# Optimization experiments

Hardware: AMD Instinct MI355X
Metric: run time of the kernel (lower is better)

## Reference

```python
import jax, jax.numpy as jnp
import numpy as np

D = 4096          # input_dim == output_dim (square FAUST factors)
N = 1024          # batch rows of U
NNZ = 131072      # nonzeros per factor (32 per row)
K = 4             # number of sparse factors


def setup_inputs() -> dict:
    key = jax.random.key(0)
    k_u, k_b, k_v, k_r, k_c = jax.random.split(key, 5)
    U = jax.random.normal(k_u, (N, D), dtype=jnp.float32)
    bias = jax.random.normal(k_b, (D,), dtype=jnp.float32)
    # glorot-ish scaling: ~32 nnz per row -> scale by 1/sqrt(32) for stable chain
    vals = jax.random.normal(k_v, (K, NNZ), dtype=jnp.float32) * (1.0 / np.sqrt(32.0))
    rows = jax.random.randint(k_r, (K, NNZ), 0, D, dtype=jnp.int32)
    cols = jax.random.randint(k_c, (K, NNZ), 0, D, dtype=jnp.int32)
    return {"U": U, "bias": bias, "vals": vals, "rows": rows, "cols": cols}


def _spmm(rows, cols, vals, X):
    # sparse (COO) [D, D] @ dense X [D, N] -> [D, N]
    return jax.ops.segment_sum(vals[:, None] * X[cols], rows, num_segments=D)


def reference(U, bias, vals, rows, cols):
    # torch code applies sparse_matrices[-1] first, then [k-2] ... [0]
    y = U.T  # [D, N]
    for i in range(K - 1, -1, -1):
        y = _spmm(rows[i], cols[i], vals[i], y)
    return y.T + bias  # [N, D]
```

## Files before the change

### kernel.cpp

```cpp
#include <hip/hip_runtime.h>

#define D_DIM 4096
#define N_DIM 1024
#define NNZ_F 131072
#define K_F 4
#define NCHUNK 8
#define LPR 16
#define RPB 16
#define MAXE 1024
#define SEGE 512
#define XS8 (N_DIM / 8)

#define T_TILES ((D_DIM / 64) * (N_DIM / 64))
#define TSTRIDE 132

__device__ __forceinline__ unsigned short f2bf(float f) {
    union { float f; unsigned int u; } v; v.f = f;
    unsigned int r = v.u + 0x7fffu + ((v.u >> 16) & 1u);
    return (unsigned short)(r >> 16);
}
__device__ __forceinline__ float bf_lo(unsigned int w) {
    return __uint_as_float(w << 16);
}
__device__ __forceinline__ float bf_hi_raw(unsigned int w) {
    return __uint_as_float(w);
}

__global__ __launch_bounds__(1024) void fused_t_build_k(const float* __restrict__ in,
                                                        unsigned short* __restrict__ outb,
                                                        const int* __restrict__ rows,
                                                        int* __restrict__ row_ptr_g,
                                                        int* __restrict__ cursor_g,
                                                        int* __restrict__ srow_g) {
    __shared__ int s_cnt[4 * D_DIM];
    __shared__ int s_part[1024];
    const int tid = threadIdx.x;
    const int bid = blockIdx.x;

    if (bid >= K_F) {
        const int tb = bid - K_F;
        float (*tile)[65] = (float (*)[65])s_cnt;
        const int gxi = tb & 63;
        const int gyi = tb >> 6;
        const int c0 = gxi * 64;
        const int r0 = gyi * 64;
        const int tx = tid & 63;
        const int ty = tid >> 6;
#pragma unroll
        for (int i = ty; i < 64; i += 16)
            tile[i][tx] = in[(size_t)(r0 + i) * D_DIM + c0 + tx];
        __syncthreads();
        const int px = (tid & 15) * 4;
        const int py = tid >> 4;
        ushort4 w;
        w.x = f2bf(tile[px + 0][py]);
        w.y = f2bf(tile[px + 1][py]);
        w.z = f2bf(tile[px + 2][py]);
        w.w = f2bf(tile[px + 3][py]);
        *(ushort4*)&outb[(size_t)(c0 + py) * N_DIM + r0 + px] = w;
        return;
    }

    const int f = bid;
    const int grp = (tid >> 8) & 3;
#pragma unroll
    for (int k = 0; k < 16; ++k) s_cnt[tid + k * 1024] = 0;
    __syncthreads();

    int* h = s_cnt + grp * D_DIM;
    const int4* rp4 = (const int4*)(rows + (size_t)f * NNZ_F);
#pragma unroll 4
    for (int it = 0; it < NNZ_F / 4096; ++it) {
        int4 r4 = rp4[(size_t)it * 1024 + tid];
        atomicAdd(&h[r4.x], 1);
        atomicAdd(&h[r4.y], 1);
        atomicAdd(&h[r4.z], 1);
        atomicAdd(&h[r4.w], 1);
    }
    __syncthreads();

    int c[4];
#pragma unroll
    for (int k = 0; k < 4; ++k)
        c[k] = s_cnt[tid * 4 + k] + s_cnt[D_DIM + tid * 4 + k]
             + s_cnt[2 * D_DIM + tid * 4 + k] + s_cnt[3 * D_DIM + tid * 4 + k];
    const int b = tid * 4;

    int* rp   = row_ptr_g + (size_t)f * (D_DIM + 1);
    int* cur  = cursor_g + (size_t)f * D_DIM;
    int* srow = srow_g + (size_t)f * D_DIM;

    if (f == 0) {
        const int part = c[0] + c[1] + c[2] + c[3];
        s_part[tid] = part;
        __syncthreads();
        for (int off = 1; off < 1024; off <<= 1) {
            int v = (tid >= off) ? s_part[tid - off] : 0;
            __syncthreads();
            s_part[tid] += v;
            __syncthreads();
        }
        int excl = s_part[tid] - part;
#pragma unroll
        for (int k = 0; k < 4; ++k) {
            rp[b + k] = excl; cur[b + k] = excl; srow[b + k] = b + k; excl += c[k];
        }
        if (tid == 1023) rp[D_DIM] = NNZ_F;
        return;
    }

    __syncthreads();
    int* hist = s_cnt + 4096;
    int* binc = s_cnt + 4352;
    int* sA   = s_cnt + 4608;
    int* sB   = s_cnt + 4864;
    if (tid < 256) { hist[tid] = 0; binc[tid] = 0; }
    __syncthreads();
#pragma unroll
    for (int k = 0; k < 4; ++k) {
        int l = c[k] > 255 ? 255 : c[k];
        atomicAdd(&hist[l], 1);
    }
    __syncthreads();
    if (tid < 256) { int hv = hist[tid]; sA[tid] = hv; sB[tid] = hv * tid; }
    __syncthreads();
    for (int off = 1; off < 256; off <<= 1) {
        int a = 0, bb = 0;
        if (tid < 256 && tid >= off) { a = sA[tid - off]; bb = sB[tid - off]; }
        __syncthreads();
        if (tid < 256) { sA[tid] += a; sB[tid] += bb; }
        __syncthreads();
    }
#pragma unroll
    for (int k = 0; k < 4; ++k) {
        const int l = c[k] > 255 ? 255 : c[k];
        const int idx = atomicAdd(&binc[l], 1);
        const int pos    = sA[l] - hist[l] + idx;
        const int startp = sB[l] - hist[l] * l + idx * l;
        srow[pos] = b + k;
        rp[pos] = startp;
        cur[b + k] = startp;
    }
    if (tid == 1023) rp[D_DIM] = NNZ_F;
}

__global__ __launch_bounds__(1024) void scatter_all_k(const int* __restrict__ rows,
                                                      const int* __restrict__ cols,
                                                      const float* __restrict__ vals,
                                                      int* __restrict__ cursor,
                                                      uint2* __restrict__ csr) {
    const int f = blockIdx.x >> 5;
    const size_t q = (size_t)(blockIdx.x & 31) * 1024 + threadIdx.x;
    const size_t base = (size_t)f * NNZ_F;
    const int4   r4 = ((const int4*)(rows + base))[q];
    const int4   c4 = ((const int4*)(cols + base))[q];
    const float4 v4 = ((const float4*)(vals + base))[q];
    int* curf = cursor + (size_t)f * D_DIM;
    int p;
    p = atomicAdd(&curf[r4.x], 1);
    csr[base + p] = make_uint2((unsigned)c4.x << 11, __float_as_uint(v4.x));
    p = atomicAdd(&curf[r4.y], 1);
    csr[base + p] = make_uint2((unsigned)c4.y << 11, __float_as_uint(v4.y));
    p = atomicAdd(&curf[r4.z], 1);
    csr[base + p] = make_uint2((unsigned)c4.z << 11, __float_as_uint(v4.z));
    p = atomicAdd(&curf[r4.w], 1);
    csr[base + p] = make_uint2((unsigned)c4.w << 11, __float_as_uint(v4.w));
}

template <bool FINAL>
__global__ __launch_bounds__(256) void spmm_chunk_k(const int* __restrict__ row_ptr,
                                                    const int* __restrict__ sorted_rows,
                                                    const uint2* __restrict__ csr,
                                                    const char* __restrict__ Xb,
                                                    uint4* __restrict__ Y,
                                                    float* __restrict__ out,
                                                    const float* __restrict__ bias) {
    constexpr int SMEM_BYTES = FINAL ? (16 * TSTRIDE * 4) : (4 * SEGE * 8);
    __shared__ __align__(16) char smem_raw[SMEM_BYTES];

    const int tid   = threadIdx.x;
    const int chunk = blockIdx.x & (NCHUNK - 1);
    const int rg    = blockIdx.x >> 3;
    const int lane  = tid & 15;
    const int slot  = chunk * LPR + lane;
    const unsigned sl16 = (unsigned)slot * 16u;

    float acc[8];
#pragma unroll
    for (int k = 0; k < 8; ++k) acc[k] = 0.f;

    if (!FINAL) {
        uint2 (*seg)[SEGE] = (uint2(*)[SEGE])smem_raw;
        const int wid  = tid >> 6;
        const int wl   = tid & 63;
        const int sub4 = (tid >> 4) & 3;
        int q;
        switch (wid) {
            case 0:  q = rg;        break;
            case 1:  q = 511 - rg;  break;
            case 2:  q = 512 + rg;  break;
            default: q = 1023 - rg; break;
        }
        const int qb    = q * 4;
        const int qs    = row_ptr[qb];
        const int qe    = row_ptr[qb + 4];
        const int start = row_ptr[qb + sub4];
        const int end_  = row_ptr[qb + sub4 + 1];
        const int r     = sorted_rows[qb + sub4];
        const int total = qe - qs;

        if (total <= SEGE) {
            for (int t = wl; t < total; t += 64)
                seg[wid][t] = csr[qs + t];
            asm volatile("s_waitcnt lgkmcnt(0)" ::: "memory");
            const uint2* sp = seg[wid];
            int j = start - qs;
            const int je = end_ - qs;
#pragma unroll 2
            for (; j + 1 < je; j += 2) {
                const uint2 e0 = sp[j];
                const uint2 e1 = sp[j + 1];
                const uint4 x0 = *(const uint4*)(Xb + (e0.x + sl16));
                const uint4 x1 = *(const uint4*)(Xb + (e1.x + sl16));
                const float v0 = __uint_as_float(e0.y);
                const float v1 = __uint_as_float(e1.y);
                acc[0] += v0 * bf_lo(x0.x); acc[1] += v0 * bf_hi_raw(x0.x);
                acc[2] += v0 * bf_lo(x0.y); acc[3] += v0 * bf_hi_raw(x0.y);
                acc[4] += v0 * bf_lo(x0.z); acc[5] += v0 * bf_hi_raw(x0.z);
                acc[6] += v0 * bf_lo(x0.w); acc[7] += v0 * bf_hi_raw(x0.w);
                acc[0] += v1 * bf_lo(x1.x); acc[1] += v1 * bf_hi_raw(x1.x);
                acc[2] += v1 * bf_lo(x1.y); acc[3] += v1 * bf_hi_raw(x1.y);
                acc[4] += v1 * bf_lo(x1.z); acc[5] += v1 * bf_hi_raw(x1.z);
                acc[6] += v1 * bf_lo(x1.w); acc[7] += v1 * bf_hi_raw(x1.w);
            }
            if (j < je) {
                const uint2 e0 = sp[j];
                const uint4 x0 = *(const uint4*)(Xb + (e0.x + sl16));
                const float v0 = __uint_as_float(e0.y);
                acc[0] += v0 * bf_lo(x0.x); acc[1] += v0 * bf_hi_raw(x0.x);
                acc[2] += v0 * bf_lo(x0.y); acc[3] += v0 * bf_hi_raw(x0.y);
                acc[4] += v0 * bf_lo(x0.z); acc[5] += v0 * bf_hi_raw(x0.z);
                acc[6] += v0 * bf_lo(x0.w); acc[7] += v0 * bf_hi_raw(x0.w);
            }
        } else {
            for (int j = start; j < end_; ++j) {
                const uint2 e0 = csr[j];
                const uint4 x0 = *(const uint4*)(Xb + (e0.x + sl16));
                const float v0 = __uint_as_float(e0.y);
                acc[0] += v0 * bf_lo(x0.x); acc[1] += v0 * bf_hi_raw(x0.x);
                acc[2] += v0 * bf_lo(x0.y); acc[3] += v0 * bf_hi_raw(x0.y);
                acc[4] += v0 * bf_lo(x0.z); acc[5] += v0 * bf_hi_raw(x0.z);
                acc[6] += v0 * bf_lo(x0.w); acc[7] += v0 * bf_hi_raw(x0.w);
            }
        }

        uint4 o;
        o.x = (unsigned int)f2bf(acc[0]) | ((unsigned int)f2bf(acc[1]) << 16);
        o.y = (unsigned int)f2bf(acc[2]) | ((unsigned int)f2bf(acc[3]) << 16);
        o.z = (unsigned int)f2bf(acc[4]) | ((unsigned int)f2bf(acc[5]) << 16);
        o.w = (unsigned int)f2bf(acc[6]) | ((unsigned int)f2bf(acc[7]) << 16);
        Y[(size_t)r * XS8 + slot] = o;
        return;
    }

    float* smem   = (float*)smem_raw;
    uint2* s_ent  = (uint2*)smem_raw;
    int*   s_ptr  = (int*)smem_raw + 2048;
    int*   s_srow = (int*)smem_raw + 2072;

    const int r0  = rg * RPB;
    const int sub = tid >> 4;

    if (tid <= RPB) s_ptr[tid] = row_ptr[r0 + tid];
    if (tid < RPB)  s_srow[tid] = sorted_rows[r0 + tid];
    __syncthreads();
    const int base  = s_ptr[0];
    const int total = s_ptr[RPB] - base;
    const int start = s_ptr[sub] - base;
    const int end_  = s_ptr[sub + 1] - base;
    const int r     = s_srow[sub];

    for (int cb2 = 0; cb2 < total; cb2 += MAXE) {
        int cnt = total - cb2;
        if (cnt > MAXE) cnt = MAXE;
        for (int t = tid; t < cnt; t += 256)
            s_ent[t] = csr[base + cb2 + t];
        __syncthreads();
        const int js = start > cb2 ? start : cb2;
        const int je = end_ < cb2 + cnt ? end_ : cb2 + cnt;
        int j = js;
#pragma unroll 2
        for (; j + 1 < je; j += 2) {
            const int j0 = j - cb2;
            const uint2 e0 = s_ent[j0];
            const uint2 e1 = s_ent[j0 + 1];
            const uint4 x0 = *(const uint4*)(Xb + (e0.x + sl16));
            const uint4 x1 = *(const uint4*)(Xb + (e1.x + sl16));
            const float v0 = __uint_as_float(e0.y);
            const float v1 = __uint_as_float(e1.y);
            acc[0] += v0 * bf_lo(x0.x); acc[1] += v0 * bf_hi_raw(x0.x);
            acc[2] += v0 * bf_lo(x0.y); acc[3] += v0 * bf_hi_raw(x0.y);
            acc[4] += v0 * bf_lo(x0.z); acc[5] += v0 * bf_hi_raw(x0.z);
            acc[6] += v0 * bf_lo(x0.w); acc[7] += v0 * bf_hi_raw(x0.w);
            acc[0] += v1 * bf_lo(x1.x); acc[1] += v1 * bf_hi_raw(x1.x);
            acc[2] += v1 * bf_lo(x1.y); acc[3] += v1 * bf_hi_raw(x1.y);
            acc[4] += v1 * bf_lo(x1.z); acc[5] += v1 * bf_hi_raw(x1.z);
            acc[6] += v1 * bf_lo(x1.w); acc[7] += v1 * bf_hi_raw(x1.w);
        }
        if (j < je) {
            const int j0 = j - cb2;
            const uint2 e0 = s_ent[j0];
            const uint4 x0 = *(const uint4*)(Xb + (e0.x + sl16));
            const float v0 = __uint_as_float(e0.y);
            acc[0] += v0 * bf_lo(x0.x); acc[1] += v0 * bf_hi_raw(x0.x);
            acc[2] += v0 * bf_lo(x0.y); acc[3] += v0 * bf_hi_raw(x0.y);
            acc[4] += v0 * bf_lo(x0.z); acc[5] += v0 * bf_hi_raw(x0.z);
            acc[6] += v0 * bf_lo(x0.w); acc[7] += v0 * bf_hi_raw(x0.w);
        }
        __syncthreads();
    }

    __syncthreads();
    float* tile = smem;
    const int wbase = sub * TSTRIDE + lane * 8;
    *(float4*)&tile[wbase]     = make_float4(acc[0], acc[1], acc[2], acc[3]);
    *(float4*)&tile[wbase + 4] = make_float4(acc[4], acc[5], acc[6], acc[7]);
    __syncthreads();
    const int n0 = chunk * (N_DIM / NCHUNK);
#pragma unroll
    for (int t = tid; t < 512; t += 256) {
        const int n_loc = t >> 2;
        const int qd    = t & 3;
        float4 o;
        o.x = tile[(qd * 4 + 0) * TSTRIDE + n_loc];
        o.y = tile[(qd * 4 + 1) * TSTRIDE + n_loc];
        o.z = tile[(qd * 4 + 2) * TSTRIDE + n_loc];
        o.w = tile[(qd * 4 + 3) * TSTRIDE + n_loc];
        const float4 bv = *(const float4*)&bias[r0 + qd * 4];
        o.x += bv.x; o.y += bv.y; o.z += bv.z; o.w += bv.w;
        *(float4*)&out[(size_t)(n0 + n_loc) * D_DIM + r0 + qd * 4] = o;
    }
}

extern "C" void kernel_launch(void* const* d_in, const int* in_sizes, int n_in,
                              void* d_out, int out_size, void* d_ws, size_t ws_size,
                              hipStream_t stream) {
    const float* U    = (const float*)d_in[0];
    const float* bias = (const float*)d_in[1];
    const float* vals = (const float*)d_in[2];
    const int*   rows = (const int*)d_in[3];
    const int*   cols = (const int*)d_in[4];
    float* out = (float*)d_out;

    char* ws = (char*)d_ws;
    size_t off = 0;
    char* bufA = ws;                   off += (size_t)D_DIM * N_DIM * 2;
    char* bufB = ws + off;             off += (size_t)D_DIM * N_DIM * 2;
    int* row_ptr = (int*)(ws + off);   off += (size_t)K_F * (D_DIM + 1) * 4;
    off = (off + 15) & ~(size_t)15;
    int* cursor  = (int*)(ws + off);   off += (size_t)K_F * D_DIM * 4;
    int* srow    = (int*)(ws + off);   off += (size_t)K_F * D_DIM * 4;
    off = (off + 15) & ~(size_t)15;
    uint2* csr   = (uint2*)(ws + off); off += (size_t)K_F * NNZ_F * 8;

    const int grid_spmm = (D_DIM / RPB) * NCHUNK;

    fused_t_build_k<<<T_TILES + K_F, 1024, 0, stream>>>(
        U, (unsigned short*)bufA, rows, row_ptr, cursor, srow);

    scatter_all_k<<<K_F * (NNZ_F / 4096), 1024, 0, stream>>>(rows, cols, vals, cursor, csr);

    spmm_chunk_k<false><<<grid_spmm, 256, 0, stream>>>(
        row_ptr + 3 * (D_DIM + 1), srow + 3 * D_DIM, csr + 3 * (size_t)NNZ_F,
        (const char*)bufA, (uint4*)bufB, nullptr, nullptr);
    spmm_chunk_k<false><<<grid_spmm, 256, 0, stream>>>(
        row_ptr + 2 * (D_DIM + 1), srow + 2 * D_DIM, csr + 2 * (size_t)NNZ_F,
        (const char*)bufB, (uint4*)bufA, nullptr, nullptr);
    spmm_chunk_k<false><<<grid_spmm, 256, 0, stream>>>(
        row_ptr + 1 * (D_DIM + 1), srow + 1 * D_DIM, csr + 1 * (size_t)NNZ_F,
        (const char*)bufA, (uint4*)bufB, nullptr, nullptr);
    spmm_chunk_k<true><<<grid_spmm, 256, 0, stream>>>(
        row_ptr + 0 * (D_DIM + 1), srow + 0 * D_DIM, csr + 0 * (size_t)NNZ_F,
        (const char*)bufB, nullptr, out, bias);
}
```

Before: 105.0 us.

## Balance final SpMM by length-sorting factor 0 quads and reuse per-wave path

Factor 0's row_ptr build now bins each group of four rows by its total length and writes the groups in length-sorted order, as the other factors already do, instead of keeping natural row order. This lets the final SpMM use the same per-wave, quad-paired, block-barrier-free path as the intermediate stages, replacing the block-wide chunked shared-memory loop with its __syncthreads. The final output is transposed through per-wave shared memory and written with the bias added for the four consecutive original rows (d0 = r - sub4). This relies on the sorted rows within a quad staying contiguous and aligned, and adds a histogram and scan step to factor 0's setup.

```diff
diff --git a/kernel.cpp b/kernel.cpp
--- a/kernel.cpp
+++ b/kernel.cpp
@@ -7,12 +7,10 @@
 #define NCHUNK 8
 #define LPR 16
 #define RPB 16
-#define MAXE 1024
 #define SEGE 512
 #define XS8 (N_DIM / 8)
 
 #define T_TILES ((D_DIM / 64) * (N_DIM / 64))
-#define TSTRIDE 132
 
 __device__ __forceinline__ unsigned short f2bf(float f) {
     union { float f; unsigned int u; } v; v.f = f;
@@ -33,7 +31,6 @@
                                                         int* __restrict__ cursor_g,
                                                         int* __restrict__ srow_g) {
     __shared__ int s_cnt[4 * D_DIM];
-    __shared__ int s_part[1024];
     const int tid = threadIdx.x;
     const int bid = blockIdx.x;
 
@@ -89,27 +86,42 @@
     int* rp   = row_ptr_g + (size_t)f * (D_DIM + 1);
     int* cur  = cursor_g + (size_t)f * D_DIM;
     int* srow = srow_g + (size_t)f * D_DIM;
+    __syncthreads();
 
     if (f == 0) {
-        const int part = c[0] + c[1] + c[2] + c[3];
-        s_part[tid] = part;
-        __syncthreads();
-        for (int off = 1; off < 1024; off <<= 1) {
-            int v = (tid >= off) ? s_part[tid - off] : 0;
+        int* hist = s_cnt + 4096;
+        int* binc = s_cnt + 4608;
+        int* sA   = s_cnt + 5120;
+        int* sB   = s_cnt + 5632;
+        if (tid < 512) { hist[tid] = 0; binc[tid] = 0; }
+        __syncthreads();
+        const int qlen = c[0] + c[1] + c[2] + c[3];
+        const int l = qlen > 511 ? 511 : qlen;
+        atomicAdd(&hist[l], 1);
+        __syncthreads();
+        if (tid < 512) { int hv = hist[tid]; sA[tid] = hv; sB[tid] = hv * tid; }
+        __syncthreads();
+        for (int off = 1; off < 512; off <<= 1) {
+            int a = 0, bb = 0;
+            if (tid < 512 && tid >= off) { a = sA[tid - off]; bb = sB[tid - off]; }
             __syncthreads();
-            s_part[tid] += v;
+            if (tid < 512) { sA[tid] += a; sB[tid] += bb; }
             __syncthreads();
         }
-        int excl = s_part[tid] - part;
+        const int idx = atomicAdd(&binc[l], 1);
+        const int pos = sA[l] - hist[l] + idx;
+        int pref = sB[l] - hist[l] * l + idx * l;
 #pragma unroll
         for (int k = 0; k < 4; ++k) {
-            rp[b + k] = excl; cur[b + k] = excl; srow[b + k] = b + k; excl += c[k];
+            rp[pos * 4 + k] = pref;
+            srow[pos * 4 + k] = b + k;
+            cur[b + k] = pref;
+            pref += c[k];
         }
         if (tid == 1023) rp[D_DIM] = NNZ_F;
         return;
     }
 
-    __syncthreads();
     int* hist = s_cnt + 4096;
     int* binc = s_cnt + 4352;
     int* sA   = s_cnt + 4608;
@@ -175,8 +187,7 @@
                                                     uint4* __restrict__ Y,
                                                     float* __restrict__ out,
                                                     const float* __restrict__ bias) {
-    constexpr int SMEM_BYTES = FINAL ? (16 * TSTRIDE * 4) : (4 * SEGE * 8);
-    __shared__ __align__(16) char smem_raw[SMEM_BYTES];
+    __shared__ __align__(16) uint2 seg[4][SEGE];
 
     const int tid   = threadIdx.x;
     const int chunk = blockIdx.x & (NCHUNK - 1);
@@ -184,116 +195,40 @@
     const int lane  = tid & 15;
     const int slot  = chunk * LPR + lane;
     const unsigned sl16 = (unsigned)slot * 16u;
+    const int wid  = tid >> 6;
+    const int wl   = tid & 63;
+    const int sub4 = (tid >> 4) & 3;
+
+    int q;
+    switch (wid) {
+        case 0:  q = rg;        break;
+        case 1:  q = 511 - rg;  break;
+        case 2:  q = 512 + rg;  break;
+        default: q = 1023 - rg; break;
+    }
+    const int qb    = q * 4;
+    const int qs    = row_ptr[qb];
+    const int qe    = row_ptr[qb + 4];
+    const int start = row_ptr[qb + sub4];
+    const int end_  = row_ptr[qb + sub4 + 1];
+    const int r     = sorted_rows[qb + sub4];
+    const int total = qe - qs;
 
     float acc[8];
 #pragma unroll
     for (int k = 0; k < 8; ++k) acc[k] = 0.f;
 
-    if (!FINAL) {
-        uint2 (*seg)[SEGE] = (uint2(*)[SEGE])smem_raw;
-        const int wid  = tid >> 6;
-        const int wl   = tid & 63;
-        const int sub4 = (tid >> 4) & 3;
-        int q;
-        switch (wid) {
-            case 0:  q = rg;        break;
-            case 1:  q = 511 - rg;  break;
-            case 2:  q = 512 + rg;  break;
-            default: q = 1023 - rg; break;
-        }
-        const int qb    = q * 4;
-        const int qs    = row_ptr[qb];
-        const int qe    = row_ptr[qb + 4];
-        const int start = row_ptr[qb + sub4];
-        const int end_  = row_ptr[qb + sub4 + 1];
-        const int r     = sorted_rows[qb + sub4];
-        const int total = qe - qs;
-
-        if (total <= SEGE) {
-            for (int t = wl; t < total; t += 64)
-                seg[wid][t] = csr[qs + t];
-            asm volatile("s_waitcnt lgkmcnt(0)" ::: "memory");
-            const uint2* sp = seg[wid];
-            int j = start - qs;
-            const int je = end_ - qs;
-#pragma unroll 2
-            for (; j + 1 < je; j += 2) {
-                const uint2 e0 = sp[j];
-                const uint2 e1 = sp[j + 1];
-                const uint4 x0 = *(const uint4*)(Xb + (e0.x + sl16));
-                const uint4 x1 = *(const uint4*)(Xb + (e1.x + sl16));
-                const float v0 = __uint_as_float(e0.y);
-                const float v1 = __uint_as_float(e1.y);
-                acc[0] += v0 * bf_lo(x0.x); acc[1] += v0 * bf_hi_raw(x0.x);
-                acc[2] += v0 * bf_lo(x0.y); acc[3] += v0 * bf_hi_raw(x0.y);
-                acc[4] += v0 * bf_lo(x0.z); acc[5] += v0 * bf_hi_raw(x0.z);
-                acc[6] += v0 * bf_lo(x0.w); acc[7] += v0 * bf_hi_raw(x0.w);
-                acc[0] += v1 * bf_lo(x1.x); acc[1] += v1 * bf_hi_raw(x1.x);
-                acc[2] += v1 * bf_lo(x1.y); acc[3] += v1 * bf_hi_raw(x1.y);
-                acc[4] += v1 * bf_lo(x1.z); acc[5] += v1 * bf_hi_raw(x1.z);
-                acc[6] += v1 * bf_lo(x1.w); acc[7] += v1 * bf_hi_raw(x1.w);
-            }
-            if (j < je) {
-                const uint2 e0 = sp[j];
-                const uint4 x0 = *(const uint4*)(Xb + (e0.x + sl16));
-                const float v0 = __uint_as_float(e0.y);
-                acc[0] += v0 * bf_lo(x0.x); acc[1] += v0 * bf_hi_raw(x0.x);
-                acc[2] += v0 * bf_lo(x0.y); acc[3] += v0 * bf_hi_raw(x0.y);
-                acc[4] += v0 * bf_lo(x0.z); acc[5] += v0 * bf_hi_raw(x0.z);
-                acc[6] += v0 * bf_lo(x0.w); acc[7] += v0 * bf_hi_raw(x0.w);
-            }
-        } else {
-            for (int j = start; j < end_; ++j) {
-                const uint2 e0 = csr[j];
-                const uint4 x0 = *(const uint4*)(Xb + (e0.x + sl16));
-                const float v0 = __uint_as_float(e0.y);
-                acc[0] += v0 * bf_lo(x0.x); acc[1] += v0 * bf_hi_raw(x0.x);
-                acc[2] += v0 * bf_lo(x0.y); acc[3] += v0 * bf_hi_raw(x0.y);
-                acc[4] += v0 * bf_lo(x0.z); acc[5] += v0 * bf_hi_raw(x0.z);
-                acc[6] += v0 * bf_lo(x0.w); acc[7] += v0 * bf_hi_raw(x0.w);
-            }
-        }
-
-        uint4 o;
-        o.x = (unsigned int)f2bf(acc[0]) | ((unsigned int)f2bf(acc[1]) << 16);
-        o.y = (unsigned int)f2bf(acc[2]) | ((unsigned int)f2bf(acc[3]) << 16);
-        o.z = (unsigned int)f2bf(acc[4]) | ((unsigned int)f2bf(acc[5]) << 16);
-        o.w = (unsigned int)f2bf(acc[6]) | ((unsigned int)f2bf(acc[7]) << 16);
-        Y[(size_t)r * XS8 + slot] = o;
-        return;
-    }
-
-    float* smem   = (float*)smem_raw;
-    uint2* s_ent  = (uint2*)smem_raw;
-    int*   s_ptr  = (int*)smem_raw + 2048;
-    int*   s_srow = (int*)smem_raw + 2072;
-
-    const int r0  = rg * RPB;
-    const int sub = tid >> 4;
-
-    if (tid <= RPB) s_ptr[tid] = row_ptr[r0 + tid];
-    if (tid < RPB)  s_srow[tid] = sorted_rows[r0 + tid];
-    __syncthreads();
-    const int base  = s_ptr[0];
-    const int total = s_ptr[RPB] - base;
-    const int start = s_ptr[sub] - base;
-    const int end_  = s_ptr[sub + 1] - base;
-    const int r     = s_srow[sub];
-
-    for (int cb2 = 0; cb2 < total; cb2 += MAXE) {
-        int cnt = total - cb2;
-        if (cnt > MAXE) cnt = MAXE;
-        for (int t = tid; t < cnt; t += 256)
-            s_ent[t] = csr[base + cb2 + t];
-        __syncthreads();
-        const int js = start > cb2 ? start : cb2;
-        const int je = end_ < cb2 + cnt ? end_ : cb2 + cnt;
-        int j = js;
+    if (total <= SEGE) {
+        for (int t = wl; t < total; t += 64)
+            seg[wid][t] = csr[qs + t];
+        asm volatile("s_waitcnt lgkmcnt(0)" ::: "memory");
+        const uint2* sp = seg[wid];
+        int j = start - qs;
+        const int je = end_ - qs;
 #pragma unroll 2
         for (; j + 1 < je; j += 2) {
-            const int j0 = j - cb2;
-            const uint2 e0 = s_ent[j0];
-            const uint2 e1 = s_ent[j0 + 1];
+            const uint2 e0 = sp[j];
+            const uint2 e1 = sp[j + 1];
             const uint4 x0 = *(const uint4*)(Xb + (e0.x + sl16));
             const uint4 x1 = *(const uint4*)(Xb + (e1.x + sl16));
             const float v0 = __uint_as_float(e0.y);
@@ -308,8 +243,7 @@
             acc[6] += v1 * bf_lo(x1.w); acc[7] += v1 * bf_hi_raw(x1.w);
         }
         if (j < je) {
-            const int j0 = j - cb2;
-            const uint2 e0 = s_ent[j0];
+            const uint2 e0 = sp[j];
             const uint4 x0 = *(const uint4*)(Xb + (e0.x + sl16));
             const float v0 = __uint_as_float(e0.y);
             acc[0] += v0 * bf_lo(x0.x); acc[1] += v0 * bf_hi_raw(x0.x);
@@ -317,28 +251,45 @@
             acc[4] += v0 * bf_lo(x0.z); acc[5] += v0 * bf_hi_raw(x0.z);
             acc[6] += v0 * bf_lo(x0.w); acc[7] += v0 * bf_hi_raw(x0.w);
         }
-        __syncthreads();
-    }
-
-    __syncthreads();
-    float* tile = smem;
-    const int wbase = sub * TSTRIDE + lane * 8;
-    *(float4*)&tile[wbase]     = make_float4(acc[0], acc[1], acc[2], acc[3]);
-    *(float4*)&tile[wbase + 4] = make_float4(acc[4], acc[5], acc[6], acc[7]);
-    __syncthreads();
+    } else {
+        for (int j = start; j < end_; ++j) {
+            const uint2 e0 = csr[j];
+            const uint4 x0 = *(const uint4*)(Xb + (e0.x + sl16));
+            const float v0 = __uint_as_float(e0.y);
+            acc[0] += v0 * bf_lo(x0.x); acc[1] += v0 * bf_hi_raw(x0.x);
+            acc[2] += v0 * bf_lo(x0.y); acc[3] += v0 * bf_hi_raw(x0.y);
+            acc[4] += v0 * bf_lo(x0.z); acc[5] += v0 * bf_hi_raw(x0.z);
+            acc[6] += v0 * bf_lo(x0.w); acc[7] += v0 * bf_hi_raw(x0.w);
+        }
+    }
+
+    if (!FINAL) {
+        uint4 o;
+        o.x = (unsigned int)f2bf(acc[0]) | ((unsigned int)f2bf(acc[1]) << 16);
+        o.y = (unsigned int)f2bf(acc[2]) | ((unsigned int)f2bf(acc[3]) << 16);
+        o.z = (unsigned int)f2bf(acc[4]) | ((unsigned int)f2bf(acc[5]) << 16);
+        o.w = (unsigned int)f2bf(acc[6]) | ((unsigned int)f2bf(acc[7]) << 16);
+        Y[(size_t)r * XS8 + slot] = o;
+        return;
+    }
+
+    float* tf = (float*)&seg[wid][0];
+    const int wbase = sub4 * 132 + lane * 8;
+    *(float4*)&tf[wbase]     = make_float4(acc[0], acc[1], acc[2], acc[3]);
+    *(float4*)&tf[wbase + 4] = make_float4(acc[4], acc[5], acc[6], acc[7]);
+    asm volatile("s_waitcnt lgkmcnt(0)" ::: "memory");
+    const int d0 = r - sub4;
     const int n0 = chunk * (N_DIM / NCHUNK);
-#pragma unroll
-    for (int t = tid; t < 512; t += 256) {
-        const int n_loc = t >> 2;
-        const int qd    = t & 3;
+    const float4 bv = *(const float4*)&bias[d0];
+#pragma unroll
+    for (int it = 0; it < 2; ++it) {
+        const int n = it * 64 + wl;
         float4 o;
-        o.x = tile[(qd * 4 + 0) * TSTRIDE + n_loc];
-        o.y = tile[(qd * 4 + 1) * TSTRIDE + n_loc];
-        o.z = tile[(qd * 4 + 2) * TSTRIDE + n_loc];
-        o.w = tile[(qd * 4 + 3) * TSTRIDE + n_loc];
-        const float4 bv = *(const float4*)&bias[r0 + qd * 4];
-        o.x += bv.x; o.y += bv.y; o.z += bv.z; o.w += bv.w;
-        *(float4*)&out[(size_t)(n0 + n_loc) * D_DIM + r0 + qd * 4] = o;
+        o.x = tf[0 * 132 + n] + bv.x;
+        o.y = tf[1 * 132 + n] + bv.y;
+        o.z = tf[2 * 132 + n] + bv.z;
+        o.w = tf[3 * 132 + n] + bv.w;
+        *(float4*)&out[(size_t)(n0 + n) * D_DIM + d0] = o;
     }
 }
 
```

Result: no change. 106.8 us (+1.7%).
